# Kernel tuning notes

Measured on AMD Instinct MI355X. Metric: run time of the kernel, lower is better.

Reference implementation:

```python
import jax, jax.numpy as jnp
import numpy as np

NUM_EXPERTS = 8
HIDDEN = 2048
INTER = 4096
TOKENS = 1024


def setup_inputs() -> dict:
    key = jax.random.key(0)
    k1, k2, k3, k4 = jax.random.split(key, 4)
    hidden_states = jax.random.normal(k1, (TOKENS, HIDDEN), dtype=jnp.float32)
    router_logits = jax.random.normal(k2, (TOKENS, NUM_EXPERTS), dtype=jnp.float32)
    # W13: fused [gate_proj; up_proj] per expert: [E, 2*I, H]
    W13 = jax.random.normal(k3, (NUM_EXPERTS, 2 * INTER, HIDDEN), dtype=jnp.float32) * (1.0 / np.sqrt(HIDDEN))
    # W2: down_proj per expert: [E, H, I]
    W2 = jax.random.normal(k4, (NUM_EXPERTS, HIDDEN, INTER), dtype=jnp.float32) * (1.0 / np.sqrt(INTER))
    return {"hidden_states": hidden_states, "router_logits": router_logits,
            "W13": W13, "W2": W2, "top_k": 2}


def reference(hidden_states, router_logits, W13, W2, top_k):
    # Mixtral-style MoE: softmax -> top_k -> renormalize -> SwiGLU experts -> weighted combine
    T, E = router_logits.shape
    probs = jax.nn.softmax(router_logits.astype(jnp.float32), axis=-1)
    topk_w, topk_idx = jax.lax.top_k(probs, top_k)          # [T, k]
    topk_w = topk_w / jnp.sum(topk_w, axis=-1, keepdims=True)  # renormalize=True
    # dense routing matrix [T, E] with zeros for unselected experts
    routing = jnp.zeros((T, E), dtype=hidden_states.dtype)
    routing = routing.at[jnp.arange(T)[:, None], topk_idx].add(topk_w.astype(hidden_states.dtype))
    # grouped gate_up GEMM: [T, E, 2I]
    gate_up = jnp.einsum('th,eoh->teo', hidden_states, W13)
    gate, up = jnp.split(gate_up, 2, axis=-1)               # each [T, E, I]
    act = jax.nn.silu(gate) * up                            # SwiGLU
    # grouped down GEMM: [T, E, H]
    expert_out = jnp.einsum('tei,ehi->teh', act, W2)
    # scatter-combine with routing weights
    return jnp.einsum('teh,te->th', expert_out, routing)
```

## Files before the change

kernel.cpp:

```cpp
#include <hip/hip_runtime.h>

#define NEXP 8
#define HID 2048
#define INTER 4096
#define NTOK 1024
#define CAP 512
#define BK 64

typedef short bf8 __attribute__((ext_vector_type(8)));
typedef float f4  __attribute__((ext_vector_type(4)));

__device__ __forceinline__ unsigned short f2bf(float f) {
  unsigned u = __builtin_bit_cast(unsigned, f);
  u += 0x7fffu + ((u >> 16) & 1u);
  return (unsigned short)(u >> 16);
}

__device__ __forceinline__ void ld_lds16(const void* g, void* l) {
  __builtin_amdgcn_global_load_lds(
      (const __attribute__((address_space(1))) unsigned*)g,
      (__attribute__((address_space(3))) unsigned*)l, 16, 0, 0);
}

__global__ void k_router(const float* __restrict__ lg, int* __restrict__ cnt,
                         int* __restrict__ tok, float* __restrict__ wgt) {
  __shared__ int lc[NEXP];
  int t = threadIdx.x;
  if (t < NEXP) lc[t] = 0;
  __syncthreads();
  float l[NEXP];
#pragma unroll
  for (int i = 0; i < NEXP; ++i) l[i] = lg[t * NEXP + i];
  int i1 = 0; float v1 = l[0];
#pragma unroll
  for (int i = 1; i < NEXP; ++i) if (l[i] > v1) { v1 = l[i]; i1 = i; }
  int i2 = -1; float v2 = -3.4e38f;
#pragma unroll
  for (int i = 0; i < NEXP; ++i) if (i != i1 && l[i] > v2) { v2 = l[i]; i2 = i; }
  float e2 = __expf(v2 - v1);
  float w1 = 1.f / (1.f + e2);
  float w2 = e2 / (1.f + e2);
  int s1 = atomicAdd(&lc[i1], 1);
  if (s1 < CAP) { tok[i1 * CAP + s1] = t; wgt[i1 * CAP + s1] = w1; }
  int s2 = atomicAdd(&lc[i2], 1);
  if (s2 < CAP) { tok[i2 * CAP + s2] = t; wgt[i2 * CAP + s2] = w2; }
  __syncthreads();
  if (t < NEXP) cnt[t] = lc[t];
}

__global__ void k_gather(const float* __restrict__ hid, const int* __restrict__ cnt,
                         const int* __restrict__ tok, unsigned short* __restrict__ hs) {
  int b = blockIdx.x;
  int e = b >> 9, s = b & (CAP - 1);
  if (s >= cnt[e]) return;
  int t = tok[e * CAP + s];
  const float4* src = (const float4*)(hid + (size_t)t * HID);
  ushort4* dst = (ushort4*)(hs + ((size_t)e * CAP + s) * HID);
  for (int i = threadIdx.x; i < HID / 4; i += 128) {
    float4 v = src[i];
    ushort4 o = make_ushort4(f2bf(v.x), f2bf(v.y), f2bf(v.z), f2bf(v.w));
    dst[i] = o;
  }
}

__global__ __launch_bounds__(256, 2) void k_gemm1(
    const unsigned short* __restrict__ hs, const float* __restrict__ W13,
    const int* __restrict__ cnt, unsigned short* __restrict__ act) {
  int e = blockIdx.x >> 7;
  int n0 = (blockIdx.x & 127) * 32;
  int count = cnt[e];
  if (count <= 0) return;
  if (count > CAP) count = CAP;

  __shared__ __align__(16) unsigned short lA[3 * 128 * BK];
  __shared__ __align__(16) unsigned short lB[64 * BK];

  int tid = threadIdx.x;
  int wv = tid >> 6, ln = tid & 63;
  int quad = ln >> 4, l16 = ln & 15;

  const unsigned short* A0 = hs + (size_t)e * CAP * HID;
  const float* B = W13 + (size_t)e * (2 * INTER) * HID;

  int r0 = tid >> 3;
  int bc = tid & 7;
  const float* g0 = B + (size_t)(n0 + r0) * HID + bc * 8;
  const float* g1 = B + (size_t)(INTER + n0 + r0) * HID + bc * 8;
  unsigned short* wp0 = &lB[r0 * BK + ((bc ^ (r0 & 7)) * 8)];
  unsigned short* wp1 = &lB[(r0 + 32) * BK + ((bc ^ (r0 & 7)) * 8)];

  for (int m0 = 0; m0 < count; m0 += 384) {
    int rem = count - m0;
    int mtLive = (rem + 127) >> 7; if (mtLive > 3) mtLive = 3;
    const unsigned short* A = A0 + (size_t)m0 * HID;

    f4 acc[3][2][2][2];
#pragma unroll
    for (int a = 0; a < 3; ++a)
#pragma unroll
      for (int b2 = 0; b2 < 2; ++b2)
#pragma unroll
        for (int c = 0; c < 2; ++c)
#pragma unroll
          for (int d = 0; d < 2; ++d) acc[a][b2][c][d] = (f4){0.f, 0.f, 0.f, 0.f};

    for (int k0 = 0; k0 < HID; k0 += BK) {
      float4 b0a = *(const float4*)(g0 + k0);
      float4 b0b = *(const float4*)(g0 + k0 + 4);
      float4 b1a = *(const float4*)(g1 + k0);
      float4 b1b = *(const float4*)(g1 + k0 + 4);
      __syncthreads();
      int nIss = mtLive * 4;
      for (int j = 0; j < nIss; ++j) {
        int rl = j * 32 + (tid >> 3);
        int cg = (tid & 7) ^ (rl & 7);
        ld_lds16(A + (size_t)rl * HID + k0 + cg * 8, &lA[j * 2048 + wv * 512]);
      }
      union { bf8 v; unsigned short u[8]; } p0, p1;
      p0.u[0] = f2bf(b0a.x); p0.u[1] = f2bf(b0a.y); p0.u[2] = f2bf(b0a.z); p0.u[3] = f2bf(b0a.w);
      p0.u[4] = f2bf(b0b.x); p0.u[5] = f2bf(b0b.y); p0.u[6] = f2bf(b0b.z); p0.u[7] = f2bf(b0b.w);
      p1.u[0] = f2bf(b1a.x); p1.u[1] = f2bf(b1a.y); p1.u[2] = f2bf(b1a.z); p1.u[3] = f2bf(b1a.w);
      p1.u[4] = f2bf(b1b.x); p1.u[5] = f2bf(b1b.y); p1.u[6] = f2bf(b1b.z); p1.u[7] = f2bf(b1b.w);
      *(bf8*)wp0 = p0.v;
      *(bf8*)wp1 = p1.v;
      __syncthreads();

#pragma unroll
      for (int ks = 0; ks < 2; ++ks) {
        int c = ks * 4 + quad;
        bf8 bg[2][2];
#pragma unroll
        for (int mat = 0; mat < 2; ++mat)
#pragma unroll
          for (int ns = 0; ns < 2; ++ns) {
            int br = mat * 32 + ns * 16 + l16;
            bg[mat][ns] = *(const bf8*)&lB[br * BK + ((c ^ (br & 7)) * 8)];
          }
#pragma unroll
        for (int mt = 0; mt < 3; ++mt) {
          if (mt >= mtLive) break;
#pragma unroll
          for (int ms = 0; ms < 2; ++ms) {
            int rl = mt * 128 + wv * 32 + ms * 16 + l16;
            bf8 a = *(const bf8*)&lA[rl * BK + ((c ^ (rl & 7)) * 8)];
#pragma unroll
            for (int mat = 0; mat < 2; ++mat)
#pragma unroll
              for (int ns = 0; ns < 2; ++ns)
                acc[mt][ms][mat][ns] = __builtin_amdgcn_mfma_f32_16x16x32_bf16(
                    a, bg[mat][ns], acc[mt][ms][mat][ns], 0, 0, 0);
          }
        }
      }
    }

    size_t actE = (size_t)e * CAP * INTER;
#pragma unroll
    for (int mt = 0; mt < 3; ++mt) {
      if (mt >= mtLive) break;
#pragma unroll
      for (int ms = 0; ms < 2; ++ms) {
        int rbase = m0 + mt * 128 + wv * 32 + ms * 16 + quad * 4;
#pragma unroll
        for (int ns = 0; ns < 2; ++ns) {
          int col = n0 + ns * 16 + l16;
#pragma unroll
          for (int r = 0; r < 4; ++r) {
            int row = rbase + r;
            if (row < count) {
              float g = acc[mt][ms][0][ns][r];
              float u = acc[mt][ms][1][ns][r];
              float sv = g / (1.f + __expf(-g)) * u;
              act[actE + (size_t)row * INTER + col] = f2bf(sv);
            }
          }
        }
      }
    }
  }
}

__global__ __launch_bounds__(256, 2) void k_gemm2(
    const unsigned short* __restrict__ act, const float* __restrict__ W2,
    const int* __restrict__ cnt, const int* __restrict__ tok,
    const float* __restrict__ wgt, float* __restrict__ out) {
  int e = blockIdx.x >> 6;
  int n0 = (blockIdx.x & 63) * 32;
  int count = cnt[e];
  if (count <= 0) return;
  if (count > CAP) count = CAP;

  __shared__ __align__(16) unsigned short lA[3 * 128 * BK];
  __shared__ __align__(16) unsigned short lB[32 * BK];

  int tid = threadIdx.x;
  int wv = tid >> 6, ln = tid & 63;
  int quad = ln >> 4, l16 = ln & 15;

  const unsigned short* A0 = act + (size_t)e * CAP * INTER;
  const float* B = W2 + (size_t)e * HID * INTER;

  int r0 = tid >> 3;
  int bc = tid & 7;
  const float* g0 = B + (size_t)(n0 + r0) * INTER + bc * 8;
  unsigned short* wp0 = &lB[r0 * BK + ((bc ^ (r0 & 7)) * 8)];

  for (int m0 = 0; m0 < count; m0 += 384) {
    int rem = count - m0;
    int mtLive = (rem + 127) >> 7; if (mtLive > 3) mtLive = 3;
    const unsigned short* A = A0 + (size_t)m0 * INTER;

    f4 acc[3][2][2];
#pragma unroll
    for (int a = 0; a < 3; ++a)
#pragma unroll
      for (int b2 = 0; b2 < 2; ++b2)
#pragma unroll
        for (int c = 0; c < 2; ++c) acc[a][b2][c] = (f4){0.f, 0.f, 0.f, 0.f};

    for (int k0 = 0; k0 < INTER; k0 += BK) {
      float4 b0a = *(const float4*)(g0 + k0);
      float4 b0b = *(const float4*)(g0 + k0 + 4);
      __syncthreads();
      int nIss = mtLive * 4;
      for (int j = 0; j < nIss; ++j) {
        int rl = j * 32 + (tid >> 3);
        int cg = (tid & 7) ^ (rl & 7);
        ld_lds16(A + (size_t)rl * INTER + k0 + cg * 8, &lA[j * 2048 + wv * 512]);
      }
      union { bf8 v; unsigned short u[8]; } p0;
      p0.u[0] = f2bf(b0a.x); p0.u[1] = f2bf(b0a.y); p0.u[2] = f2bf(b0a.z); p0.u[3] = f2bf(b0a.w);
      p0.u[4] = f2bf(b0b.x); p0.u[5] = f2bf(b0b.y); p0.u[6] = f2bf(b0b.z); p0.u[7] = f2bf(b0b.w);
      *(bf8*)wp0 = p0.v;
      __syncthreads();

#pragma unroll
      for (int ks = 0; ks < 2; ++ks) {
        int c = ks * 4 + quad;
        bf8 bb[2];
#pragma unroll
        for (int ns = 0; ns < 2; ++ns) {
          int br = ns * 16 + l16;
          bb[ns] = *(const bf8*)&lB[br * BK + ((c ^ (br & 7)) * 8)];
        }
#pragma unroll
        for (int mt = 0; mt < 3; ++mt) {
          if (mt >= mtLive) break;
#pragma unroll
          for (int ms = 0; ms < 2; ++ms) {
            int rl = mt * 128 + wv * 32 + ms * 16 + l16;
            bf8 a = *(const bf8*)&lA[rl * BK + ((c ^ (rl & 7)) * 8)];
#pragma unroll
            for (int ns = 0; ns < 2; ++ns)
              acc[mt][ms][ns] = __builtin_amdgcn_mfma_f32_16x16x32_bf16(
                  a, bb[ns], acc[mt][ms][ns], 0, 0, 0);
          }
        }
      }
    }

#pragma unroll
    for (int mt = 0; mt < 3; ++mt) {
      if (mt >= mtLive) break;
#pragma unroll
      for (int ms = 0; ms < 2; ++ms) {
        int rbase = m0 + mt * 128 + wv * 32 + ms * 16 + quad * 4;
#pragma unroll
        for (int ns = 0; ns < 2; ++ns) {
          int col = n0 + ns * 16 + l16;
#pragma unroll
          for (int r = 0; r < 4; ++r) {
            int row = rbase + r;
            if (row < count) {
              int t = tok[e * CAP + row];
              float w = wgt[e * CAP + row];
              atomicAdd(out + (size_t)t * HID + col, w * acc[mt][ms][ns][r]);
            }
          }
        }
      }
    }
  }
}

extern "C" void kernel_launch(void* const* d_in, const int* in_sizes, int n_in,
                              void* d_out, int out_size, void* d_ws, size_t ws_size,
                              hipStream_t stream) {
  const float* hidden = (const float*)d_in[0];
  const float* logits = (const float*)d_in[1];
  const float* W13    = (const float*)d_in[2];
  const float* W2     = (const float*)d_in[3];
  float* out = (float*)d_out;

  char* wsb = (char*)d_ws;
  int*   cnt = (int*)wsb;
  int*   tok = (int*)(wsb + 256);
  float* wgt = (float*)(wsb + 256 + NEXP * CAP * 4);
  unsigned short* hs  = (unsigned short*)(wsb + 256 + NEXP * CAP * 8);
  unsigned short* actb = hs + (size_t)NEXP * CAP * HID;

  hipMemsetAsync(d_out, 0, (size_t)out_size * sizeof(float), stream);
  k_router<<<1, 1024, 0, stream>>>(logits, cnt, tok, wgt);
  k_gather<<<NEXP * CAP, 128, 0, stream>>>(hidden, cnt, tok, hs);
  k_gemm1<<<NEXP * 128, 256, 0, stream>>>(hs, W13, cnt, actb);
  k_gemm2<<<NEXP * 64, 256, 0, stream>>>(actb, W2, cnt, tok, wgt, out);
}
```

Baseline: 995.7 us.

## Software-pipeline W loads with double-buffered B tile and explicit waitcnt scheduling

Both expert GEMMs now prefetch the next fp32 weight tile into registers one iteration ahead and double-buffer the bf16 B tile in LDS, using explicit vmcnt waits and raw s_barrier instead of __syncthreads. This hides global weight-load latency behind the MFMA loop. setprio raises wave priority during the MFMA section. The A tile is still single-buffered and loaded after the barrier, so its latency is only partly hidden, and the hand-placed waitcnt counts make correctness depend on the exact number of outstanding loads.

```diff
diff --git a/kernel.cpp b/kernel.cpp
--- a/kernel.cpp
+++ b/kernel.cpp
@@ -7,6 +7,8 @@
 #define CAP 512
 #define BK 64
 
+#define FENCE() do { asm volatile("" ::: "memory"); __builtin_amdgcn_sched_barrier(0); } while (0)
+
 typedef short bf8 __attribute__((ext_vector_type(8)));
 typedef float f4  __attribute__((ext_vector_type(4)));
 
@@ -20,6 +22,13 @@
   __builtin_amdgcn_global_load_lds(
       (const __attribute__((address_space(1))) unsigned*)g,
       (__attribute__((address_space(3))) unsigned*)l, 16, 0, 0);
+}
+
+__device__ __forceinline__ void packB8(unsigned short* dst, float4 a, float4 b) {
+  union { bf8 v; unsigned short u[8]; } p;
+  p.u[0] = f2bf(a.x); p.u[1] = f2bf(a.y); p.u[2] = f2bf(a.z); p.u[3] = f2bf(a.w);
+  p.u[4] = f2bf(b.x); p.u[5] = f2bf(b.y); p.u[6] = f2bf(b.z); p.u[7] = f2bf(b.w);
+  *(bf8*)dst = p.v;
 }
 
 __global__ void k_router(const float* __restrict__ lg, int* __restrict__ cnt,
@@ -73,7 +82,7 @@
   if (count > CAP) count = CAP;
 
   __shared__ __align__(16) unsigned short lA[3 * 128 * BK];
-  __shared__ __align__(16) unsigned short lB[64 * BK];
+  __shared__ __align__(16) unsigned short lB[2][64 * BK];
 
   int tid = threadIdx.x;
   int wv = tid >> 6, ln = tid & 63;
@@ -86,12 +95,13 @@
   int bc = tid & 7;
   const float* g0 = B + (size_t)(n0 + r0) * HID + bc * 8;
   const float* g1 = B + (size_t)(INTER + n0 + r0) * HID + bc * 8;
-  unsigned short* wp0 = &lB[r0 * BK + ((bc ^ (r0 & 7)) * 8)];
-  unsigned short* wp1 = &lB[(r0 + 32) * BK + ((bc ^ (r0 & 7)) * 8)];
+  int wpo0 = r0 * BK + ((bc ^ (r0 & 7)) * 8);
+  int wpo1 = (r0 + 32) * BK + ((bc ^ (r0 & 7)) * 8);
 
   for (int m0 = 0; m0 < count; m0 += 384) {
     int rem = count - m0;
     int mtLive = (rem + 127) >> 7; if (mtLive > 3) mtLive = 3;
+    int nIss = mtLive * 4;
     const unsigned short* A = A0 + (size_t)m0 * HID;
 
     f4 acc[3][2][2][2];
@@ -104,27 +114,33 @@
 #pragma unroll
           for (int d = 0; d < 2; ++d) acc[a][b2][c][d] = (f4){0.f, 0.f, 0.f, 0.f};
 
-    for (int k0 = 0; k0 < HID; k0 += BK) {
-      float4 b0a = *(const float4*)(g0 + k0);
-      float4 b0b = *(const float4*)(g0 + k0 + 4);
-      float4 b1a = *(const float4*)(g1 + k0);
-      float4 b1b = *(const float4*)(g1 + k0 + 4);
-      __syncthreads();
-      int nIss = mtLive * 4;
-      for (int j = 0; j < nIss; ++j) {
-        int rl = j * 32 + (tid >> 3);
-        int cg = (tid & 7) ^ (rl & 7);
-        ld_lds16(A + (size_t)rl * HID + k0 + cg * 8, &lA[j * 2048 + wv * 512]);
-      }
-      union { bf8 v; unsigned short u[8]; } p0, p1;
-      p0.u[0] = f2bf(b0a.x); p0.u[1] = f2bf(b0a.y); p0.u[2] = f2bf(b0a.z); p0.u[3] = f2bf(b0a.w);
-      p0.u[4] = f2bf(b0b.x); p0.u[5] = f2bf(b0b.y); p0.u[6] = f2bf(b0b.z); p0.u[7] = f2bf(b0b.w);
-      p1.u[0] = f2bf(b1a.x); p1.u[1] = f2bf(b1a.y); p1.u[2] = f2bf(b1a.z); p1.u[3] = f2bf(b1a.w);
-      p1.u[4] = f2bf(b1b.x); p1.u[5] = f2bf(b1b.y); p1.u[6] = f2bf(b1b.z); p1.u[7] = f2bf(b1b.w);
-      *(bf8*)wp0 = p0.v;
-      *(bf8*)wp1 = p1.v;
-      __syncthreads();
-
+    float4 c0 = *(const float4*)(g0 + 0);
+    float4 c1 = *(const float4*)(g0 + 4);
+    float4 c2 = *(const float4*)(g1 + 0);
+    float4 c3 = *(const float4*)(g1 + 4);
+    FENCE();
+    for (int j = 0; j < nIss; ++j) {
+      int rl = j * 32 + (tid >> 3);
+      int cg = (tid & 7) ^ (rl & 7);
+      ld_lds16(A + (size_t)rl * HID + cg * 8, &lA[j * 2048 + wv * 512]);
+    }
+    FENCE();
+    packB8(&lB[0][wpo0], c0, c1);
+    packB8(&lB[0][wpo1], c2, c3);
+    c0 = *(const float4*)(g0 + BK);
+    c1 = *(const float4*)(g0 + BK + 4);
+    c2 = *(const float4*)(g1 + BK);
+    c3 = *(const float4*)(g1 + BK + 4);
+    FENCE();
+    asm volatile("s_waitcnt vmcnt(4) lgkmcnt(0)" ::: "memory");
+    __builtin_amdgcn_sched_barrier(0);
+    __builtin_amdgcn_s_barrier();
+    FENCE();
+
+    int kb = 0;
+    for (int k0 = 0; k0 < HID; k0 += BK, kb ^= 1) {
+      const unsigned short* lBk = lB[kb];
+      __builtin_amdgcn_s_setprio(1);
 #pragma unroll
       for (int ks = 0; ks < 2; ++ks) {
         int c = ks * 4 + quad;
@@ -134,7 +150,7 @@
 #pragma unroll
           for (int ns = 0; ns < 2; ++ns) {
             int br = mat * 32 + ns * 16 + l16;
-            bg[mat][ns] = *(const bf8*)&lB[br * BK + ((c ^ (br & 7)) * 8)];
+            bg[mat][ns] = *(const bf8*)&lBk[br * BK + ((c ^ (br & 7)) * 8)];
           }
 #pragma unroll
         for (int mt = 0; mt < 3; ++mt) {
@@ -151,6 +167,30 @@
                     a, bg[mat][ns], acc[mt][ms][mat][ns], 0, 0, 0);
           }
         }
+      }
+      __builtin_amdgcn_s_setprio(0);
+      FENCE();
+      __builtin_amdgcn_s_barrier();
+      FENCE();
+      if (k0 + BK < HID) {
+        packB8(&lB[kb ^ 1][wpo0], c0, c1);
+        packB8(&lB[kb ^ 1][wpo1], c2, c3);
+        for (int j = 0; j < nIss; ++j) {
+          int rl = j * 32 + (tid >> 3);
+          int cg = (tid & 7) ^ (rl & 7);
+          ld_lds16(A + (size_t)rl * HID + (k0 + BK) + cg * 8, &lA[j * 2048 + wv * 512]);
+        }
+        FENCE();
+        int kn = (k0 + 2 * BK < HID) ? (k0 + 2 * BK) : 0;
+        c0 = *(const float4*)(g0 + kn);
+        c1 = *(const float4*)(g0 + kn + 4);
+        c2 = *(const float4*)(g1 + kn);
+        c3 = *(const float4*)(g1 + kn + 4);
+        FENCE();
+        asm volatile("s_waitcnt vmcnt(4) lgkmcnt(0)" ::: "memory");
+        __builtin_amdgcn_sched_barrier(0);
+        __builtin_amdgcn_s_barrier();
+        FENCE();
       }
     }
 
@@ -191,7 +231,7 @@
   if (count > CAP) count = CAP;
 
   __shared__ __align__(16) unsigned short lA[3 * 128 * BK];
-  __shared__ __align__(16) unsigned short lB[32 * BK];
+  __shared__ __align__(16) unsigned short lB[2][32 * BK];
 
   int tid = threadIdx.x;
   int wv = tid >> 6, ln = tid & 63;
@@ -203,11 +243,12 @@
   int r0 = tid >> 3;
   int bc = tid & 7;
   const float* g0 = B + (size_t)(n0 + r0) * INTER + bc * 8;
-  unsigned short* wp0 = &lB[r0 * BK + ((bc ^ (r0 & 7)) * 8)];
+  int wpo0 = r0 * BK + ((bc ^ (r0 & 7)) * 8);
 
   for (int m0 = 0; m0 < count; m0 += 384) {
     int rem = count - m0;
     int mtLive = (rem + 127) >> 7; if (mtLive > 3) mtLive = 3;
+    int nIss = mtLive * 4;
     const unsigned short* A = A0 + (size_t)m0 * INTER;
 
     f4 acc[3][2][2];
@@ -218,22 +259,28 @@
 #pragma unroll
         for (int c = 0; c < 2; ++c) acc[a][b2][c] = (f4){0.f, 0.f, 0.f, 0.f};
 
-    for (int k0 = 0; k0 < INTER; k0 += BK) {
-      float4 b0a = *(const float4*)(g0 + k0);
-      float4 b0b = *(const float4*)(g0 + k0 + 4);
-      __syncthreads();
-      int nIss = mtLive * 4;
-      for (int j = 0; j < nIss; ++j) {
-        int rl = j * 32 + (tid >> 3);
-        int cg = (tid & 7) ^ (rl & 7);
-        ld_lds16(A + (size_t)rl * INTER + k0 + cg * 8, &lA[j * 2048 + wv * 512]);
-      }
-      union { bf8 v; unsigned short u[8]; } p0;
-      p0.u[0] = f2bf(b0a.x); p0.u[1] = f2bf(b0a.y); p0.u[2] = f2bf(b0a.z); p0.u[3] = f2bf(b0a.w);
-      p0.u[4] = f2bf(b0b.x); p0.u[5] = f2bf(b0b.y); p0.u[6] = f2bf(b0b.z); p0.u[7] = f2bf(b0b.w);
-      *(bf8*)wp0 = p0.v;
-      __syncthreads();
-
+    float4 c0 = *(const float4*)(g0 + 0);
+    float4 c1 = *(const float4*)(g0 + 4);
+    FENCE();
+    for (int j = 0; j < nIss; ++j) {
+      int rl = j * 32 + (tid >> 3);
+      int cg = (tid & 7) ^ (rl & 7);
+      ld_lds16(A + (size_t)rl * INTER + cg * 8, &lA[j * 2048 + wv * 512]);
+    }
+    FENCE();
+    packB8(&lB[0][wpo0], c0, c1);
+    c0 = *(const float4*)(g0 + BK);
+    c1 = *(const float4*)(g0 + BK + 4);
+    FENCE();
+    asm volatile("s_waitcnt vmcnt(2) lgkmcnt(0)" ::: "memory");
+    __builtin_amdgcn_sched_barrier(0);
+    __builtin_amdgcn_s_barrier();
+    FENCE();
+
+    int kb = 0;
+    for (int k0 = 0; k0 < INTER; k0 += BK, kb ^= 1) {
+      const unsigned short* lBk = lB[kb];
+      __builtin_amdgcn_s_setprio(1);
 #pragma unroll
       for (int ks = 0; ks < 2; ++ks) {
         int c = ks * 4 + quad;
@@ -241,7 +288,7 @@
 #pragma unroll
         for (int ns = 0; ns < 2; ++ns) {
           int br = ns * 16 + l16;
-          bb[ns] = *(const bf8*)&lB[br * BK + ((c ^ (br & 7)) * 8)];
+          bb[ns] = *(const bf8*)&lBk[br * BK + ((c ^ (br & 7)) * 8)];
         }
 #pragma unroll
         for (int mt = 0; mt < 3; ++mt) {
@@ -256,6 +303,27 @@
                   a, bb[ns], acc[mt][ms][ns], 0, 0, 0);
           }
         }
+      }
+      __builtin_amdgcn_s_setprio(0);
+      FENCE();
+      __builtin_amdgcn_s_barrier();
+      FENCE();
+      if (k0 + BK < INTER) {
+        packB8(&lB[kb ^ 1][wpo0], c0, c1);
+        for (int j = 0; j < nIss; ++j) {
+          int rl = j * 32 + (tid >> 3);
+          int cg = (tid & 7) ^ (rl & 7);
+          ld_lds16(A + (size_t)rl * INTER + (k0 + BK) + cg * 8, &lA[j * 2048 + wv * 512]);
+        }
+        FENCE();
+        int kn = (k0 + 2 * BK < INTER) ? (k0 + 2 * BK) : 0;
+        c0 = *(const float4*)(g0 + kn);
+        c1 = *(const float4*)(g0 + kn + 4);
+        FENCE();
+        asm volatile("s_waitcnt vmcnt(2) lgkmcnt(0)" ::: "memory");
+        __builtin_amdgcn_sched_barrier(0);
+        __builtin_amdgcn_s_barrier();
+        FENCE();
       }
     }
 
```

Measured after the change: 988.6 us. Within noise of the previous version (-0.7%).
